# Kernel optimization log

Hardware: AMD Instinct MI355X
Metric: run time of the kernel (lower is better)

The kernel has to match this reference:

```python
import jax, jax.numpy as jnp
import numpy as np

B, IN, H = 16384, 512, 512
EPS = 1e-5


def _layernorm(x, g, b):
    mu = jnp.mean(x, axis=-1, keepdims=True)
    var = jnp.mean(jnp.square(x - mu), axis=-1, keepdims=True)
    return (x - mu) * jax.lax.rsqrt(var + EPS) * g + b


def setup_inputs() -> dict:
    key = jax.random.key(0)
    ks = jax.random.split(key, 16)
    lim_in = 1.0 / np.sqrt(IN)
    lim_h = 1.0 / np.sqrt(H)

    def lin(kw, kb, fan_in, lim):
        W = jax.random.uniform(kw, (H, fan_in), jnp.float32, -lim, lim)
        b = jax.random.uniform(kb, (H,), jnp.float32, -lim, lim)
        return W, b

    Wz, bz = lin(ks[0], ks[1], IN, lim_in)
    Uz, buz = lin(ks[2], ks[3], H, lim_h)
    Wr, br = lin(ks[4], ks[5], IN, lim_in)
    Ur, bur = lin(ks[6], ks[7], H, lim_h)
    Wh, bh = lin(ks[8], ks[9], IN, lim_in)
    Uh, buh = lin(ks[10], ks[11], H, lim_h)

    return {
        "x": jax.random.normal(ks[12], (B, IN), jnp.float32),
        "h": jax.random.normal(ks[13], (B, H), jnp.float32),
        "Wz": Wz, "bz": bz, "Uz": Uz, "buz": buz,
        "Wr": Wr, "br": br, "Ur": Ur, "bur": bur,
        "Wh": Wh, "bh": bh, "Uh": Uh, "buh": buh,
        "ln_g": jnp.ones((3, H), jnp.float32),
        "ln_b": jnp.zeros((3, H), jnp.float32),
    }


def reference(x, h, Wz, bz, Uz, buz, Wr, br, Ur, bur, Wh, bh, Uh, buh, ln_g, ln_b):
    # six small linears (torch nn.Linear: x @ W.T + b)
    z_pre = jnp.einsum('bi,hi->bh', x, Wz) + bz + jnp.einsum('bj,hj->bh', h, Uz) + buz
    r_pre = jnp.einsum('bi,hi->bh', x, Wr) + br + jnp.einsum('bj,hj->bh', h, Ur) + bur
    # NOTE: original applies pre-norm, pre-sigmoid r to uh(h)
    hh_pre = jnp.einsum('bi,hi->bh', x, Wh) + bh + r_pre * (jnp.einsum('bj,hj->bh', h, Uh) + buh)
    z = jax.nn.sigmoid(_layernorm(z_pre, ln_g[0], ln_b[0]))
    h_hat = jnp.tan(_layernorm(hh_pre, ln_g[2], ln_b[2]))  # torch.tan in original (bug kept)
    return z * h + (1.0 - z) * h_hat
```

## Files before the change

kernel.cpp:

```cpp
#pragma clang fp contract(off)
#include <hip/hip_runtime.h>
#include <math.h>


#define TPB 512
typedef float f32x2 __attribute__((ext_vector_type(2)));

__device__ __forceinline__ f32x2 pkfma(f32x2 a, float bscalar, f32x2 c) {
    f32x2 b; b.x = bscalar; b.y = bscalar;
    return __builtin_elementwise_fma(a, b, c);
}

__device__ __forceinline__ float pw_avx512_128(const float* a) {
    float L[16];
#pragma unroll
    for (int l = 0; l < 16; ++l)
        L[l] = ((a[l] + a[16 + l]) + (a[32 + l] + a[48 + l]))
             + ((a[64 + l] + a[80 + l]) + (a[96 + l] + a[112 + l]));
    float s[8];
#pragma unroll
    for (int i = 0; i < 8; ++i) s[i] = L[i] + L[i + 8];
    float q[4];
#pragma unroll
    for (int i = 0; i < 4; ++i) q[i] = s[i] + s[i + 4];
    return (q[0] + q[2]) + (q[1] + q[3]);
}
__device__ float np_row_sum512(const float* a) {
    return (pw_avx512_128(a) + pw_avx512_128(a + 128))
         + (pw_avx512_128(a + 256) + pw_avx512_128(a + 384));
}

__global__ __launch_bounds__(256) void k_tr(
    const float* __restrict__ Wr, const float* __restrict__ Ur,
    const float* __restrict__ Uh, const float* __restrict__ Wh,
    const float* __restrict__ Wz, const float* __restrict__ Uz,
    float* __restrict__ P)
{
    const int idx = blockIdx.x * 256 + threadIdx.x;
    const int m = idx >> 16;
    const int t = idx & 65535;
    const int k4 = t >> 9, j = t & 511;
    const float* W = (m == 0) ? Wr : (m == 1) ? Ur : (m == 2) ? Uh
                   : (m == 3) ? Wh : (m == 4) ? Wz : Uz;
    const float4 v = *(const float4*)(W + ((size_t)j << 9) + (k4 << 2));
    *(float4*)(P + ((size_t)m << 18) + (k4 << 11) + (j << 2)) = v;
}

__global__ __launch_bounds__(TPB) void gru_fast(
    const float* __restrict__ x,  const float* __restrict__ h,
    const float* __restrict__ P,
    const float* __restrict__ bz, const float* __restrict__ buz,
    const float* __restrict__ br, const float* __restrict__ bur,
    const float* __restrict__ bh, const float* __restrict__ buh,
    const float* __restrict__ ln_g, const float* __restrict__ ln_b,
    float* __restrict__ out)
{
    __shared__ union {
        struct { float xs2[8][1024]; float hs2[8][1024]; } a;
        struct { float hha[16][516]; float lnB[16][4];
                 float zsum[16][8]; float zsq[16][8];
                 float mu[16]; float rstd[16]; float muz[16]; float rstdz[16]; } b;
    } L;

    const int j  = threadIdx.x;
    const int r0 = blockIdx.x * 16;

    {
        const float4* xg = (const float4*)(x + ((size_t)r0 << 9));
        const float4* hg = (const float4*)(h + ((size_t)r0 << 9));
        for (int i = j; i < 2048; i += TPB) {
            const int row = i >> 7, c4 = i & 127;
            const int rp = row >> 1, half = row & 1;
            const int base = rp * 1024 + c4 * 8 + half;
            const float4 vx = xg[i];
            float* xd = &L.a.xs2[0][0];
            xd[base + 0] = vx.x; xd[base + 2] = vx.y;
            xd[base + 4] = vx.z; xd[base + 6] = vx.w;
            const float4 vh = hg[i];
            float* hd = &L.a.hs2[0][0];
            hd[base + 0] = vh.x; hd[base + 2] = vh.y;
            hd[base + 4] = vh.z; hd[base + 6] = vh.w;
        }
    }
    __syncthreads();

    const float* pWr = P;
    const float* pUr = P + 262144;
    const float* pUh = P + 524288;
    const float* pWh = P + 786432;
    const float* pWz = P + 1048576;
    const float* pUz = P + 1310720;

    const float brj = br[j], burj = bur[j], buhj = buh[j], bhj = bh[j];
    const float bzj = bz[j] + buz[j];

    float hh[16], zp[16];

#pragma unroll
    for (int rh = 0; rh < 2; ++rh) {
        f32x2 aWr[4], aUr[4], aUh[4], aWh[4], aZ[4];
#pragma unroll
        for (int p = 0; p < 4; ++p) {
            aWr[p] = (f32x2)0.f; aUr[p] = (f32x2)0.f; aUh[p] = (f32x2)0.f;
            aWh[p] = (f32x2)0.f; aZ[p]  = (f32x2)0.f;
        }

        const int off0 = (j << 2);
        float4 wr = *(const float4*)(pWr + off0);
        float4 ur = *(const float4*)(pUr + off0);
        float4 uh = *(const float4*)(pUh + off0);
        float4 wh = *(const float4*)(pWh + off0);
        float4 wz = *(const float4*)(pWz + off0);
        float4 uz = *(const float4*)(pUz + off0);

#pragma unroll 2
        for (int k4 = 0; k4 < 128; ++k4) {
            const int kn = (k4 < 127) ? (k4 + 1) : 127;
            const int noff = (kn << 11) + (j << 2);
            const float4 nwr = *(const float4*)(pWr + noff);
            const float4 nur = *(const float4*)(pUr + noff);
            const float4 nuh = *(const float4*)(pUh + noff);
            const float4 nwh = *(const float4*)(pWh + noff);
            const float4 nwz = *(const float4*)(pWz + noff);
            const float4 nuz = *(const float4*)(pUz + noff);
#pragma unroll
            for (int p = 0; p < 4; ++p) {
                const int rp = rh * 4 + p;
                const float* xb = &L.a.xs2[rp][k4 << 3];
                const float* hb = &L.a.hs2[rp][k4 << 3];
                const float4 xA = *(const float4*)(xb);
                const float4 xB = *(const float4*)(xb + 4);
                const float4 hA = *(const float4*)(hb);
                const float4 hB = *(const float4*)(hb + 4);
                f32x2 x0; x0.x = xA.x; x0.y = xA.y;
                f32x2 x1; x1.x = xA.z; x1.y = xA.w;
                f32x2 x2; x2.x = xB.x; x2.y = xB.y;
                f32x2 x3; x3.x = xB.z; x3.y = xB.w;
                f32x2 h0; h0.x = hA.x; h0.y = hA.y;
                f32x2 h1; h1.x = hA.z; h1.y = hA.w;
                f32x2 h2; h2.x = hB.x; h2.y = hB.y;
                f32x2 h3; h3.x = hB.z; h3.y = hB.w;
                aWr[p] = pkfma(x0, wr.x, aWr[p]); aWr[p] = pkfma(x1, wr.y, aWr[p]);
                aWr[p] = pkfma(x2, wr.z, aWr[p]); aWr[p] = pkfma(x3, wr.w, aWr[p]);
                aUr[p] = pkfma(h0, ur.x, aUr[p]); aUr[p] = pkfma(h1, ur.y, aUr[p]);
                aUr[p] = pkfma(h2, ur.z, aUr[p]); aUr[p] = pkfma(h3, ur.w, aUr[p]);
                aUh[p] = pkfma(h0, uh.x, aUh[p]); aUh[p] = pkfma(h1, uh.y, aUh[p]);
                aUh[p] = pkfma(h2, uh.z, aUh[p]); aUh[p] = pkfma(h3, uh.w, aUh[p]);
                aWh[p] = pkfma(x0, wh.x, aWh[p]); aWh[p] = pkfma(x1, wh.y, aWh[p]);
                aWh[p] = pkfma(x2, wh.z, aWh[p]); aWh[p] = pkfma(x3, wh.w, aWh[p]);
                aZ[p]  = pkfma(x0, wz.x, aZ[p]);  aZ[p]  = pkfma(x1, wz.y, aZ[p]);
                aZ[p]  = pkfma(x2, wz.z, aZ[p]);  aZ[p]  = pkfma(x3, wz.w, aZ[p]);
                aZ[p]  = pkfma(h0, uz.x, aZ[p]);  aZ[p]  = pkfma(h1, uz.y, aZ[p]);
                aZ[p]  = pkfma(h2, uz.z, aZ[p]);  aZ[p]  = pkfma(h3, uz.w, aZ[p]);
            }
            wr = nwr; ur = nur; uh = nuh; wh = nwh; wz = nwz; uz = nuz;
        }
#pragma unroll
        for (int p = 0; p < 4; ++p) {
            const int row = (rh * 4 + p) * 2;
#pragma unroll
            for (int half = 0; half < 2; ++half) {
                const float dWr = half ? aWr[p].y : aWr[p].x;
                const float dUr = half ? aUr[p].y : aUr[p].x;
                const float dUh = half ? aUh[p].y : aUh[p].x;
                const float dWh = half ? aWh[p].y : aWh[p].x;
                const float dZ  = half ? aZ[p].y  : aZ[p].x;
                const float rp2 = ((dWr + brj) + dUr) + burj;
                const float up  = dUh + buhj;
                hh[row + half] = (dWh + bhj) + rp2 * up;
                zp[row + half] = dZ + bzj;
            }
        }
    }
    __syncthreads();

#pragma unroll
    for (int r = 0; r < 16; ++r) L.b.hha[r][j] = hh[r];
    {
        const int wid = j >> 6, lane = j & 63;
#pragma unroll
        for (int r = 0; r < 16; ++r) {
            float s = zp[r], q = zp[r] * zp[r];
#pragma unroll
            for (int o = 1; o < 64; o <<= 1) { s += __shfl_xor(s, o); q += __shfl_xor(q, o); }
            if (lane == 0) { L.b.zsum[r][wid] = s; L.b.zsq[r][wid] = q; }
        }
    }
    __syncthreads();

    if (j < 64) {
        const int r = j >> 2, b = j & 3;
        L.b.lnB[r][b] = pw_avx512_128(&L.b.hha[r][b * 128]);
    } else if (j < 80) {
        const int r = j - 64;
        float s = 0.f, q = 0.f;
#pragma unroll
        for (int w = 0; w < 8; ++w) { s += L.b.zsum[r][w]; q += L.b.zsq[r][w]; }
        const float m = s / 512.0f;
        L.b.muz[r]   = m;
        L.b.rstdz[r] = 1.0f / sqrtf(q / 512.0f - m * m + 1e-5f);
    }
    __syncthreads();
    if (j < 16) {
        const float sum = (L.b.lnB[j][0] + L.b.lnB[j][1])
                        + (L.b.lnB[j][2] + L.b.lnB[j][3]);
        L.b.mu[j] = sum / 512.0f;
    }
    __syncthreads();
#pragma unroll
    for (int r = 0; r < 16; ++r) {
        const float d = hh[r] - L.b.mu[r];
        L.b.hha[r][j] = d * d;
    }
    __syncthreads();
    if (j < 64) {
        const int r = j >> 2, b = j & 3;
        L.b.lnB[r][b] = pw_avx512_128(&L.b.hha[r][b * 128]);
    }
    __syncthreads();
    if (j < 16) {
        const float var = ((L.b.lnB[j][0] + L.b.lnB[j][1])
                         + (L.b.lnB[j][2] + L.b.lnB[j][3])) / 512.0f;
        const float ve  = var + 1e-5f;
        L.b.rstd[j] = (float)(1.0 / sqrt((double)ve));
    }
    __syncthreads();

    const float g2 = ln_g[1024 + j], b2 = ln_b[1024 + j];
    const float g0 = ln_g[j],        b0 = ln_b[j];
#pragma unroll
    for (int r = 0; r < 16; ++r) {
        const float d  = hh[r] - L.b.mu[r];
        const float t  = d * L.b.rstd[r];
        const float v  = (t * g2) + b2;
        const float th = (float)tan((double)v);
        const float vz = ((zp[r] - L.b.muz[r]) * L.b.rstdz[r]) * g0 + b0;
        const float zf = 1.0f / (1.0f + expf(-vz));
        const float hv = h[((size_t)(r0 + r) << 9) + j];
        out[((size_t)(r0 + r) << 9) + j] = (zf * hv) + (1.0f - zf) * th;
    }
}

__device__ __forceinline__ void sweep3c(const float* __restrict__ sa,
                                        const float* __restrict__ wA,
                                        const float* __restrict__ wB,
                                        const float* __restrict__ wC,
                                        float& dA, float& dB, float& dC)
{
    float a = 0.f, b = 0.f, c = 0.f;
    for (int k4 = 0; k4 < 128; ++k4) {
        const int k0 = k4 << 2;
        const float4 xv = *(const float4*)(sa + k0);
        const float4 av = *(const float4*)(wA + k0);
        const float4 bv = *(const float4*)(wB + k0);
        const float4 cv = *(const float4*)(wC + k0);
        a = fmaf(xv.x, av.x, a); a = fmaf(xv.y, av.y, a);
        a = fmaf(xv.z, av.z, a); a = fmaf(xv.w, av.w, a);
        b = fmaf(xv.x, bv.x, b); b = fmaf(xv.y, bv.y, b);
        b = fmaf(xv.z, bv.z, b); b = fmaf(xv.w, bv.w, b);
        c = fmaf(xv.x, cv.x, c); c = fmaf(xv.y, cv.y, c);
        c = fmaf(xv.z, cv.z, c); c = fmaf(xv.w, cv.w, c);
    }
    dA = a; dB = b; dC = c;
}

__global__ __launch_bounds__(TPB) void gru_np19(
    const float* __restrict__ x,  const float* __restrict__ h,
    const float* __restrict__ Wz, const float* __restrict__ bz,
    const float* __restrict__ Uz, const float* __restrict__ buz,
    const float* __restrict__ Wr, const float* __restrict__ br,
    const float* __restrict__ Ur, const float* __restrict__ bur,
    const float* __restrict__ Wh, const float* __restrict__ bh,
    const float* __restrict__ Uh, const float* __restrict__ buh,
    const float* __restrict__ ln_g, const float* __restrict__ ln_b,
    float* __restrict__ out)
{
    __shared__ union {
        float xh[2][16][512];
        struct { float hha[16][522]; float mu[16]; float rstd[16]; } ln;
    } S;
    const int tid = threadIdx.x;
    const int r = tid >> 5, jt = tid & 31;
    const int r0 = blockIdx.x * 16;
    {
        const float4* xg = (const float4*)(x + ((size_t)r0 << 9));
        const float4* hg = (const float4*)(h + ((size_t)r0 << 9));
        float4* xd = (float4*)S.xh[0];
        float4* hd = (float4*)S.xh[1];
        for (int idx = tid; idx < 2048; idx += TPB) { xd[idx] = xg[idx]; hd[idx] = hg[idx]; }
    }
    __syncthreads();
    const float* xs = S.xh[0][r];
    const float* hs = S.xh[1][r];
    float hh[16], zp[16];
    for (int jj = 0; jj < 16; ++jj) {
        const int j = jt * 16 + jj;
        const size_t jb = (size_t)j << 9;
        float dWr, dWh, zx;
        sweep3c(xs, Wr + jb, Wh + jb, Wz + jb, dWr, dWh, zx);
        float dUr, dUh, zh;
        sweep3c(hs, Ur + jb, Uh + jb, Uz + jb, dUr, dUh, zh);
        const float rp = ((dWr + br[j]) + dUr) + bur[j];
        const float up = dUh + buh[j];
        hh[jj] = (dWh + bh[j]) + rp * up;
        zp[jj] = ((zx + zh) + bz[j]) + buz[j];
    }
    __syncthreads();
    for (int jj = 0; jj < 16; ++jj) S.ln.hha[r][jt * 16 + jj] = hh[jj];
    __syncthreads();
    if (tid < 16) {
        float* a = S.ln.hha[tid];
        const float mu = np_row_sum512(a) / 512.0f;
        for (int k = 0; k < 512; ++k) { const float d = a[k] - mu; a[k] = d * d; }
        const float var = np_row_sum512(a) / 512.0f;
        const float ve  = var + 1e-5f;
        S.ln.mu[tid] = mu;
        S.ln.rstd[tid] = (float)(1.0 / sqrt((double)ve));
    }
    float sz = 0.f;
    for (int jj = 0; jj < 16; ++jj) sz += zp[jj];
#pragma unroll
    for (int off = 1; off < 32; off <<= 1) sz += __shfl_xor(sz, off, 32);
    const float muz = sz / 512.0f;
    float tz = 0.f;
    for (int jj = 0; jj < 16; ++jj) { const float d = zp[jj] - muz; tz = fmaf(d, d, tz); }
#pragma unroll
    for (int off = 1; off < 32; off <<= 1) tz += __shfl_xor(tz, off, 32);
    const float rstdz = 1.0f / sqrtf(tz / 512.0f + 1e-5f);
    __syncthreads();
    const float mu = S.ln.mu[r], rstd = S.ln.rstd[r];
    const float* hrow = h + ((size_t)(r0 + r) << 9);
    float* orow = out + ((size_t)(r0 + r) << 9);
    for (int jj = 0; jj < 16; ++jj) {
        const int j = jt * 16 + jj;
        const float d = hh[jj] - mu;
        const float v = ((d * rstd) * ln_g[1024 + j]) + ln_b[1024 + j];
        const float th = (float)tan((double)v);
        const float vz = ((zp[jj] - muz) * rstdz) * ln_g[j] + ln_b[j];
        const float zf = 1.0f / (1.0f + expf(-vz));
        orow[j] = (zf * hrow[j]) + (1.0f - zf) * th;
    }
}

extern "C" void kernel_launch(void* const* d_in, const int* in_sizes, int n_in,
                              void* d_out, int out_size, void* d_ws, size_t ws_size,
                              hipStream_t stream)
{
    (void)in_sizes; (void)n_in; (void)out_size;
    const float* x   = (const float*)d_in[0];
    const float* h   = (const float*)d_in[1];
    const float* Wz  = (const float*)d_in[2];
    const float* bz  = (const float*)d_in[3];
    const float* Uz  = (const float*)d_in[4];
    const float* buz = (const float*)d_in[5];
    const float* Wr  = (const float*)d_in[6];
    const float* br  = (const float*)d_in[7];
    const float* Ur  = (const float*)d_in[8];
    const float* bur = (const float*)d_in[9];
    const float* Wh  = (const float*)d_in[10];
    const float* bh  = (const float*)d_in[11];
    const float* Uh  = (const float*)d_in[12];
    const float* buh = (const float*)d_in[13];
    const float* lng = (const float*)d_in[14];
    const float* lnb = (const float*)d_in[15];
    float* out = (float*)d_out;

    if (ws_size >= (size_t)6 * 262144 * 4) {
        float* P = (float*)d_ws;
        hipLaunchKernelGGL(k_tr, dim3(1536), dim3(256), 0, stream,
                           Wr, Ur, Uh, Wh, Wz, Uz, P);
        hipLaunchKernelGGL(gru_fast, dim3(16384 / 16), dim3(TPB), 0, stream,
                           x, h, P, bz, buz, br, bur, bh, buh, lng, lnb, out);
    } else {
        hipLaunchKernelGGL(gru_np19, dim3(16384 / 16), dim3(TPB), 0, stream,
                           x, h, Wz, bz, Uz, buz, Wr, br, Ur, bur,
                           Wh, bh, Uh, buh, lng, lnb, out);
    }
}
```

Measured before the change: 794.3 us.

## Halve rows per block and use inline-asm packed FMA with op_sel broadcast

```diff
diff --git a/kernel.cpp b/kernel.cpp
--- a/kernel.cpp
+++ b/kernel.cpp
@@ -5,10 +5,15 @@
 
 #define TPB 512
 typedef float f32x2 __attribute__((ext_vector_type(2)));
-
-__device__ __forceinline__ f32x2 pkfma(f32x2 a, float bscalar, f32x2 c) {
-    f32x2 b; b.x = bscalar; b.y = bscalar;
-    return __builtin_elementwise_fma(a, b, c);
+typedef float f32x4 __attribute__((ext_vector_type(4)));
+
+__device__ __forceinline__ void pkfma_lo(f32x2& acc, f32x2 a, f32x2 w) {
+    asm("v_pk_fma_f32 %0, %1, %2, %0 op_sel:[0,0,0] op_sel_hi:[1,0,1]"
+        : "+v"(acc) : "v"(a), "v"(w));
+}
+__device__ __forceinline__ void pkfma_hi(f32x2& acc, f32x2 a, f32x2 w) {
+    asm("v_pk_fma_f32 %0, %1, %2, %0 op_sel:[0,1,0] op_sel_hi:[1,1,1]"
+        : "+v"(acc) : "v"(a), "v"(w));
 }
 
 __device__ __forceinline__ float pw_avx512_128(const float* a) {
@@ -56,19 +61,19 @@
     float* __restrict__ out)
 {
     __shared__ union {
-        struct { float xs2[8][1024]; float hs2[8][1024]; } a;
-        struct { float hha[16][516]; float lnB[16][4];
-                 float zsum[16][8]; float zsq[16][8];
-                 float mu[16]; float rstd[16]; float muz[16]; float rstdz[16]; } b;
+        struct { float xs2[4][1024]; float hs2[4][1024]; } a;
+        struct { float hha[8][516]; float lnB[8][4];
+                 float zsum[8][8]; float zsq[8][8];
+                 float mu[8]; float rstd[8]; float muz[8]; float rstdz[8]; } b;
     } L;
 
     const int j  = threadIdx.x;
-    const int r0 = blockIdx.x * 16;
+    const int r0 = blockIdx.x * 8;
 
     {
         const float4* xg = (const float4*)(x + ((size_t)r0 << 9));
         const float4* hg = (const float4*)(h + ((size_t)r0 << 9));
-        for (int i = j; i < 2048; i += TPB) {
+        for (int i = j; i < 1024; i += TPB) {
             const int row = i >> 7, c4 = i & 127;
             const int rp = row >> 1, half = row & 1;
             const int base = rp * 1024 + c4 * 8 + half;
@@ -94,92 +99,100 @@
     const float brj = br[j], burj = bur[j], buhj = buh[j], bhj = bh[j];
     const float bzj = bz[j] + buz[j];
 
-    float hh[16], zp[16];
-
-#pragma unroll
-    for (int rh = 0; rh < 2; ++rh) {
-        f32x2 aWr[4], aUr[4], aUh[4], aWh[4], aZ[4];
+    f32x2 aWr[4], aUr[4], aUh[4], aWh[4], aZ[4];
+#pragma unroll
+    for (int p = 0; p < 4; ++p) {
+        aWr[p] = (f32x2)0.f; aUr[p] = (f32x2)0.f; aUh[p] = (f32x2)0.f;
+        aWh[p] = (f32x2)0.f; aZ[p]  = (f32x2)0.f;
+    }
+
+    const int off0 = (j << 2);
+    f32x4 wr = *(const f32x4*)(pWr + off0);
+    f32x4 ur = *(const f32x4*)(pUr + off0);
+    f32x4 uh = *(const f32x4*)(pUh + off0);
+    f32x4 wh = *(const f32x4*)(pWh + off0);
+    f32x4 wz = *(const f32x4*)(pWz + off0);
+    f32x4 uz = *(const f32x4*)(pUz + off0);
+
+#pragma unroll 2
+    for (int k4 = 0; k4 < 128; ++k4) {
+        const int kn = (k4 < 127) ? (k4 + 1) : 127;
+        const int noff = (kn << 11) + (j << 2);
+        const f32x4 nwr = *(const f32x4*)(pWr + noff);
+        const f32x4 nur = *(const f32x4*)(pUr + noff);
+        const f32x4 nuh = *(const f32x4*)(pUh + noff);
+        const f32x4 nwh = *(const f32x4*)(pWh + noff);
+        const f32x4 nwz = *(const f32x4*)(pWz + noff);
+        const f32x4 nuz = *(const f32x4*)(pUz + noff);
+
+        const f32x2 wrA = __builtin_shufflevector(wr, wr, 0, 1);
+        const f32x2 wrB = __builtin_shufflevector(wr, wr, 2, 3);
+        const f32x2 urA = __builtin_shufflevector(ur, ur, 0, 1);
+        const f32x2 urB = __builtin_shufflevector(ur, ur, 2, 3);
+        const f32x2 uhA = __builtin_shufflevector(uh, uh, 0, 1);
+        const f32x2 uhB = __builtin_shufflevector(uh, uh, 2, 3);
+        const f32x2 whA = __builtin_shufflevector(wh, wh, 0, 1);
+        const f32x2 whB = __builtin_shufflevector(wh, wh, 2, 3);
+        const f32x2 wzA = __builtin_shufflevector(wz, wz, 0, 1);
+        const f32x2 wzB = __builtin_shufflevector(wz, wz, 2, 3);
+        const f32x2 uzA = __builtin_shufflevector(uz, uz, 0, 1);
+        const f32x2 uzB = __builtin_shufflevector(uz, uz, 2, 3);
 #pragma unroll
         for (int p = 0; p < 4; ++p) {
-            aWr[p] = (f32x2)0.f; aUr[p] = (f32x2)0.f; aUh[p] = (f32x2)0.f;
-            aWh[p] = (f32x2)0.f; aZ[p]  = (f32x2)0.f;
+            const float* xb = &L.a.xs2[p][k4 << 3];
+            const float* hb = &L.a.hs2[p][k4 << 3];
+            const f32x4 xA = *(const f32x4*)(xb);
+            const f32x4 xB = *(const f32x4*)(xb + 4);
+            const f32x4 hA = *(const f32x4*)(hb);
+            const f32x4 hB = *(const f32x4*)(hb + 4);
+            const f32x2 x0 = __builtin_shufflevector(xA, xA, 0, 1);
+            const f32x2 x1 = __builtin_shufflevector(xA, xA, 2, 3);
+            const f32x2 x2 = __builtin_shufflevector(xB, xB, 0, 1);
+            const f32x2 x3 = __builtin_shufflevector(xB, xB, 2, 3);
+            const f32x2 h0 = __builtin_shufflevector(hA, hA, 0, 1);
+            const f32x2 h1 = __builtin_shufflevector(hA, hA, 2, 3);
+            const f32x2 h2 = __builtin_shufflevector(hB, hB, 0, 1);
+            const f32x2 h3 = __builtin_shufflevector(hB, hB, 2, 3);
+            pkfma_lo(aWr[p], x0, wrA); pkfma_hi(aWr[p], x1, wrA);
+            pkfma_lo(aWr[p], x2, wrB); pkfma_hi(aWr[p], x3, wrB);
+            pkfma_lo(aUr[p], h0, urA); pkfma_hi(aUr[p], h1, urA);
+            pkfma_lo(aUr[p], h2, urB); pkfma_hi(aUr[p], h3, urB);
+            pkfma_lo(aUh[p], h0, uhA); pkfma_hi(aUh[p], h1, uhA);
+            pkfma_lo(aUh[p], h2, uhB); pkfma_hi(aUh[p], h3, uhB);
+            pkfma_lo(aWh[p], x0, whA); pkfma_hi(aWh[p], x1, whA);
+            pkfma_lo(aWh[p], x2, whB); pkfma_hi(aWh[p], x3, whB);
+            pkfma_lo(aZ[p],  x0, wzA); pkfma_hi(aZ[p],  x1, wzA);
+            pkfma_lo(aZ[p],  x2, wzB); pkfma_hi(aZ[p],  x3, wzB);
+            pkfma_lo(aZ[p],  h0, uzA); pkfma_hi(aZ[p],  h1, uzA);
+            pkfma_lo(aZ[p],  h2, uzB); pkfma_hi(aZ[p],  h3, uzB);
         }
-
-        const int off0 = (j << 2);
-        float4 wr = *(const float4*)(pWr + off0);
-        float4 ur = *(const float4*)(pUr + off0);
-        float4 uh = *(const float4*)(pUh + off0);
-        float4 wh = *(const float4*)(pWh + off0);
-        float4 wz = *(const float4*)(pWz + off0);
-        float4 uz = *(const float4*)(pUz + off0);
-
-#pragma unroll 2
-        for (int k4 = 0; k4 < 128; ++k4) {
-            const int kn = (k4 < 127) ? (k4 + 1) : 127;
-            const int noff = (kn << 11) + (j << 2);
-            const float4 nwr = *(const float4*)(pWr + noff);
-            const float4 nur = *(const float4*)(pUr + noff);
-            const float4 nuh = *(const float4*)(pUh + noff);
-            const float4 nwh = *(const float4*)(pWh + noff);
-            const float4 nwz = *(const float4*)(pWz + noff);
-            const float4 nuz = *(const float4*)(pUz + noff);
-#pragma unroll
-            for (int p = 0; p < 4; ++p) {
-                const int rp = rh * 4 + p;
-                const float* xb = &L.a.xs2[rp][k4 << 3];
-                const float* hb = &L.a.hs2[rp][k4 << 3];
-                const float4 xA = *(const float4*)(xb);
-                const float4 xB = *(const float4*)(xb + 4);
-                const float4 hA = *(const float4*)(hb);
-                const float4 hB = *(const float4*)(hb + 4);
-                f32x2 x0; x0.x = xA.x; x0.y = xA.y;
-                f32x2 x1; x1.x = xA.z; x1.y = xA.w;
-                f32x2 x2; x2.x = xB.x; x2.y = xB.y;
-                f32x2 x3; x3.x = xB.z; x3.y = xB.w;
-                f32x2 h0; h0.x = hA.x; h0.y = hA.y;
-                f32x2 h1; h1.x = hA.z; h1.y = hA.w;
-                f32x2 h2; h2.x = hB.x; h2.y = hB.y;
-                f32x2 h3; h3.x = hB.z; h3.y = hB.w;
-                aWr[p] = pkfma(x0, wr.x, aWr[p]); aWr[p] = pkfma(x1, wr.y, aWr[p]);
-                aWr[p] = pkfma(x2, wr.z, aWr[p]); aWr[p] = pkfma(x3, wr.w, aWr[p]);
-                aUr[p] = pkfma(h0, ur.x, aUr[p]); aUr[p] = pkfma(h1, ur.y, aUr[p]);
-                aUr[p] = pkfma(h2, ur.z, aUr[p]); aUr[p] = pkfma(h3, ur.w, aUr[p]);
-                aUh[p] = pkfma(h0, uh.x, aUh[p]); aUh[p] = pkfma(h1, uh.y, aUh[p]);
-                aUh[p] = pkfma(h2, uh.z, aUh[p]); aUh[p] = pkfma(h3, uh.w, aUh[p]);
-                aWh[p] = pkfma(x0, wh.x, aWh[p]); aWh[p] = pkfma(x1, wh.y, aWh[p]);
-                aWh[p] = pkfma(x2, wh.z, aWh[p]); aWh[p] = pkfma(x3, wh.w, aWh[p]);
-                aZ[p]  = pkfma(x0, wz.x, aZ[p]);  aZ[p]  = pkfma(x1, wz.y, aZ[p]);
-                aZ[p]  = pkfma(x2, wz.z, aZ[p]);  aZ[p]  = pkfma(x3, wz.w, aZ[p]);
-                aZ[p]  = pkfma(h0, uz.x, aZ[p]);  aZ[p]  = pkfma(h1, uz.y, aZ[p]);
-                aZ[p]  = pkfma(h2, uz.z, aZ[p]);  aZ[p]  = pkfma(h3, uz.w, aZ[p]);
-            }
-            wr = nwr; ur = nur; uh = nuh; wh = nwh; wz = nwz; uz = nuz;
+        wr = nwr; ur = nur; uh = nuh; wh = nwh; wz = nwz; uz = nuz;
+    }
+
+    float hh[8], zp[8];
+#pragma unroll
+    for (int p = 0; p < 4; ++p) {
+#pragma unroll
+        for (int half = 0; half < 2; ++half) {
+            const float dWr = half ? aWr[p].y : aWr[p].x;
+            const float dUr = half ? aUr[p].y : aUr[p].x;
+            const float dUh = half ? aUh[p].y : aUh[p].x;
+            const float dWh = half ? aWh[p].y : aWh[p].x;
+            const float dZ  = half ? aZ[p].y  : aZ[p].x;
+            const float rp2 = ((dWr + brj) + dUr) + burj;
+            const float up  = dUh + buhj;
+            hh[p * 2 + half] = (dWh + bhj) + rp2 * up;
+            zp[p * 2 + half] = dZ + bzj;
         }
-#pragma unroll
-        for (int p = 0; p < 4; ++p) {
-            const int row = (rh * 4 + p) * 2;
-#pragma unroll
-            for (int half = 0; half < 2; ++half) {
-                const float dWr = half ? aWr[p].y : aWr[p].x;
-                const float dUr = half ? aUr[p].y : aUr[p].x;
-                const float dUh = half ? aUh[p].y : aUh[p].x;
-                const float dWh = half ? aWh[p].y : aWh[p].x;
-                const float dZ  = half ? aZ[p].y  : aZ[p].x;
-                const float rp2 = ((dWr + brj) + dUr) + burj;
-                const float up  = dUh + buhj;
-                hh[row + half] = (dWh + bhj) + rp2 * up;
-                zp[row + half] = dZ + bzj;
-            }
-        }
-    }
-    __syncthreads();
-
-#pragma unroll
-    for (int r = 0; r < 16; ++r) L.b.hha[r][j] = hh[r];
+    }
+    __syncthreads();
+
+#pragma unroll
+    for (int r = 0; r < 8; ++r) L.b.hha[r][j] = hh[r];
     {
         const int wid = j >> 6, lane = j & 63;
 #pragma unroll
-        for (int r = 0; r < 16; ++r) {
+        for (int r = 0; r < 8; ++r) {
             float s = zp[r], q = zp[r] * zp[r];
 #pragma unroll
             for (int o = 1; o < 64; o <<= 1) { s += __shfl_xor(s, o); q += __shfl_xor(q, o); }
@@ -188,11 +201,11 @@
     }
     __syncthreads();
 
-    if (j < 64) {
+    if (j < 32) {
         const int r = j >> 2, b = j & 3;
         L.b.lnB[r][b] = pw_avx512_128(&L.b.hha[r][b * 128]);
-    } else if (j < 80) {
-        const int r = j - 64;
+    } else if (j < 40) {
+        const int r = j - 32;
         float s = 0.f, q = 0.f;
 #pragma unroll
         for (int w = 0; w < 8; ++w) { s += L.b.zsum[r][w]; q += L.b.zsq[r][w]; }
@@ -201,24 +214,24 @@
         L.b.rstdz[r] = 1.0f / sqrtf(q / 512.0f - m * m + 1e-5f);
     }
     __syncthreads();
-    if (j < 16) {
+    if (j < 8) {
         const float sum = (L.b.lnB[j][0] + L.b.lnB[j][1])
                         + (L.b.lnB[j][2] + L.b.lnB[j][3]);
         L.b.mu[j] = sum / 512.0f;
     }
     __syncthreads();
 #pragma unroll
-    for (int r = 0; r < 16; ++r) {
+    for (int r = 0; r < 8; ++r) {
         const float d = hh[r] - L.b.mu[r];
         L.b.hha[r][j] = d * d;
     }
     __syncthreads();
-    if (j < 64) {
+    if (j < 32) {
         const int r = j >> 2, b = j & 3;
         L.b.lnB[r][b] = pw_avx512_128(&L.b.hha[r][b * 128]);
     }
     __syncthreads();
-    if (j < 16) {
+    if (j < 8) {
         const float var = ((L.b.lnB[j][0] + L.b.lnB[j][1])
                          + (L.b.lnB[j][2] + L.b.lnB[j][3])) / 512.0f;
         const float ve  = var + 1e-5f;
@@ -229,7 +242,7 @@
     const float g2 = ln_g[1024 + j], b2 = ln_b[1024 + j];
     const float g0 = ln_g[j],        b0 = ln_b[j];
 #pragma unroll
-    for (int r = 0; r < 16; ++r) {
+    for (int r = 0; r < 8; ++r) {
         const float d  = hh[r] - L.b.mu[r];
         const float t  = d * L.b.rstd[r];
         const float v  = (t * g2) + b2;
@@ -369,7 +382,7 @@
         float* P = (float*)d_ws;
         hipLaunchKernelGGL(k_tr, dim3(1536), dim3(256), 0, stream,
                            Wr, Ur, Uh, Wh, Wz, Uz, P);
-        hipLaunchKernelGGL(gru_fast, dim3(16384 / 16), dim3(TPB), 0, stream,
+        hipLaunchKernelGGL(gru_fast, dim3(16384 / 8), dim3(TPB), 0, stream,
                            x, h, P, bz, buz, br, bur, bh, buh, lng, lnb, out);
     } else {
         hipLaunchKernelGGL(gru_np19, dim3(16384 / 16), dim3(TPB), 0, stream,
```

Result: slower. 996.0 us (+25.4%).
